# Performance work log

Measured on AMD Instinct MI355X. Metric: run time of the kernel, lower is better.

The kernel has to match this reference:

```python
import jax, jax.numpy as jnp
import numpy as np

B, D, U = 4096, 2048, 2048

def setup_inputs() -> dict:
    key = jax.random.key(0)
    ks = jax.random.split(key, 16)
    s_in = 1.0 / np.sqrt(D)
    s_h = 1.0 / np.sqrt(U)
    inp = {
        "x": jax.random.normal(ks[0], (B, D), jnp.float32),
        "h": jax.random.normal(ks[1], (B, U), jnp.float32),
        "c": jax.random.normal(ks[2], (B, U), jnp.float32),
        # input-to-gate weights (Dense with bias)
        "Wxf": jax.random.normal(ks[3], (D, U), jnp.float32) * s_in,
        "Wxi": jax.random.normal(ks[4], (D, U), jnp.float32) * s_in,
        "Wxo": jax.random.normal(ks[5], (D, U), jnp.float32) * s_in,
        "Wxg": jax.random.normal(ks[6], (D, U), jnp.float32) * s_in,
        "bf": jnp.zeros((U,), jnp.float32),
        "bi": jnp.zeros((U,), jnp.float32),
        "bo": jnp.zeros((U,), jnp.float32),
        "bg": jnp.zeros((U,), jnp.float32),
        # hidden-to-gate weights (no bias)
        "Whf": jax.random.normal(ks[7], (U, U), jnp.float32) * s_h,
        "Whi": jax.random.normal(ks[8], (U, U), jnp.float32) * s_h,
        "Who": jax.random.normal(ks[9], (U, U), jnp.float32) * s_h,
        "Whg": jax.random.normal(ks[10], (U, U), jnp.float32) * s_h,
    }
    return inp

def reference(x, h, c, Wxf, Wxi, Wxo, Wxg, bf, bi, bo, bg, Whf, Whi, Who, Whg):
    # Fuse the 8 small GEMMs into two batched GEMMs over concatenated weights,
    # then one elementwise gate-fusion pass. Math identical to per-Dense form.
    Wx = jnp.concatenate([Wxf, Wxi, Wxo, Wxg], axis=1)   # [D, 4U]
    Wh = jnp.concatenate([Whf, Whi, Who, Whg], axis=1)   # [U, 4U]
    b = jnp.concatenate([bf, bi, bo, bg], axis=0)        # [4U]
    z = x @ Wx + h @ Wh + b                               # [B, 4U]
    zf, zi, zo, zg = jnp.split(z, 4, axis=1)
    f = jax.nn.sigmoid(zf)
    i = jax.nn.sigmoid(zi)
    o = jax.nn.sigmoid(zo)
    g = jnp.tanh(zg)
    c_new = f * c + i * g
    h_new = o * jnp.tanh(c_new)
    return (h_new, c_new)
```

## Files before the change

### kernel.cpp

```cpp
#include <hip/hip_runtime.h>
#include <hip/hip_bf16.h>
#include <stdint.h>

#define B_ 4096
#define D_ 2048
#define U_ 2048
#define K_ 4096
#define N_ 8192

typedef __bf16 bf16x8 __attribute__((ext_vector_type(8)));
typedef float floatx4 __attribute__((ext_vector_type(4)));

__device__ __forceinline__ unsigned short f2bf(float f) {
    union { float f; unsigned int u; } v; v.f = f;
    unsigned int u = v.u;
    unsigned int r = (u + 0x7fffu + ((u >> 16) & 1u)) >> 16;
    return (unsigned short)r;
}

__device__ __forceinline__ float bf2f(unsigned short b) {
    union { unsigned int u; float f; } v;
    v.u = ((unsigned int)b) << 16;
    return v.f;
}

__global__ void k_convA(const float* __restrict__ x, const float* __restrict__ h,
                        unsigned short* __restrict__ Abf) {
    int t = blockIdx.x * blockDim.x + threadIdx.x;
    long e = (long)t * 4;
    int b = (int)(e >> 12);
    int k = (int)(e & 4095);
    const float* src = (k < D_) ? (x + (size_t)b * D_ + k)
                                : (h + (size_t)b * U_ + (k - D_));
    float4 v = *(const float4*)src;
    ushort4 o;
    o.x = f2bf(v.x); o.y = f2bf(v.y); o.z = f2bf(v.z); o.w = f2bf(v.w);
    *(ushort4*)(Abf + e) = o;
}

__global__ void k_convB(const float* __restrict__ Wx0, const float* __restrict__ Wx1,
                        const float* __restrict__ Wx2, const float* __restrict__ Wx3,
                        const float* __restrict__ Wh0, const float* __restrict__ Wh1,
                        const float* __restrict__ Wh2, const float* __restrict__ Wh3,
                        unsigned short* __restrict__ Bt) {
    __shared__ float tile[32][33];
    int g  = blockIdx.z;
    int k0 = blockIdx.x * 32;
    int u0 = blockIdx.y * 32;
    const float* W;
    if (k0 < D_) {
        W = (g == 0 ? Wx0 : g == 1 ? Wx1 : g == 2 ? Wx2 : Wx3) + (size_t)k0 * U_;
    } else {
        W = (g == 0 ? Wh0 : g == 1 ? Wh1 : g == 2 ? Wh2 : Wh3) + (size_t)(k0 - D_) * U_;
    }
    int tx = threadIdx.x & 31, ty = threadIdx.x >> 5;
    #pragma unroll
    for (int j = 0; j < 4; ++j)
        tile[ty + 8 * j][tx] = W[(size_t)(ty + 8 * j) * U_ + u0 + tx];
    __syncthreads();
    #pragma unroll
    for (int j = 0; j < 4; ++j) {
        int u = u0 + ty + 8 * j;
        Bt[(size_t)(g * U_ + u) * K_ + k0 + tx] = f2bf(tile[tx][ty + 8 * j]);
    }
}

__device__ __forceinline__ void gload16(const unsigned short* g, unsigned short* l) {
    __builtin_amdgcn_global_load_lds(
        (const __attribute__((address_space(1))) void*)g,
        (__attribute__((address_space(3))) void*)l, 16, 0, 0);
}

__global__ __launch_bounds__(256) void k_gemm(const unsigned short* __restrict__ A,
                                              const unsigned short* __restrict__ Bt,
                                              unsigned short* __restrict__ Z) {
    __shared__ __align__(16) unsigned short As[128 * 32];
    __shared__ __align__(16) unsigned short Bs[128 * 32];
    const int m0  = blockIdx.y * 128;
    const int n0  = blockIdx.x * 128;
    const int tid = threadIdx.x;
    const int w   = tid >> 6;
    const int l   = tid & 63;

    const unsigned short* gA = A  + (size_t)(m0 + w * 16 + (l >> 2)) * K_ + (l & 3) * 8;
    const unsigned short* gB = Bt + (size_t)(n0 + w * 16 + (l >> 2)) * K_ + (l & 3) * 8;
    unsigned short* lA = As + w * 512;
    unsigned short* lB = Bs + w * 512;

    const int r     = l & 15;
    const int quad  = l >> 4;
    const int m_off = (w & 1) * 64;
    const int n_off = (w >> 1) * 64;

    floatx4 acc[4][4];
    #pragma unroll
    for (int i = 0; i < 4; ++i)
        #pragma unroll
        for (int j = 0; j < 4; ++j)
            #pragma unroll
            for (int e = 0; e < 4; ++e) acc[i][j][e] = 0.f;

    for (int k0 = 0; k0 < K_; k0 += 32) {
        __syncthreads();
        gload16(gA + k0,                  lA);
        gload16(gA + k0 + (size_t)64 * K_, lA + 2048);
        gload16(gB + k0,                  lB);
        gload16(gB + k0 + (size_t)64 * K_, lB + 2048);
        __syncthreads();

        bf16x8 af[4], bfv[4];
        #pragma unroll
        for (int i = 0; i < 4; ++i)
            af[i] = *(const bf16x8*)(As + ((m_off + i * 16 + r) * 32 + quad * 8));
        #pragma unroll
        for (int j = 0; j < 4; ++j)
            bfv[j] = *(const bf16x8*)(Bs + ((n_off + j * 16 + r) * 32 + quad * 8));
        #pragma unroll
        for (int i = 0; i < 4; ++i)
            #pragma unroll
            for (int j = 0; j < 4; ++j)
                acc[i][j] = __builtin_amdgcn_mfma_f32_16x16x32_bf16(
                    af[i], bfv[j], acc[i][j], 0, 0, 0);
    }

    #pragma unroll
    for (int i = 0; i < 4; ++i) {
        #pragma unroll
        for (int j = 0; j < 4; ++j) {
            int col = n0 + n_off + j * 16 + r;
            #pragma unroll
            for (int e = 0; e < 4; ++e) {
                int row = m0 + m_off + i * 16 + quad * 4 + e;
                Z[(size_t)row * N_ + col] = f2bf(acc[i][j][e]);
            }
        }
    }
}

__device__ __forceinline__ float sigmoidf_(float x) { return 1.0f / (1.0f + expf(-x)); }

__global__ void k_gates(const unsigned short* __restrict__ Z, const float* __restrict__ c,
                        const float* __restrict__ bfp, const float* __restrict__ bip,
                        const float* __restrict__ bop, const float* __restrict__ bgp,
                        float* __restrict__ hout, float* __restrict__ cout) {
    int t = blockIdx.x * blockDim.x + threadIdx.x;
    long e = (long)t * 4;
    int b = (int)(e >> 11);
    int u = (int)(e & 2047);
    const size_t zr = (size_t)b * N_;
    ushort4 zf4 = *(const ushort4*)(Z + zr + u);
    ushort4 zi4 = *(const ushort4*)(Z + zr + U_ + u);
    ushort4 zo4 = *(const ushort4*)(Z + zr + 2 * U_ + u);
    ushort4 zg4 = *(const ushort4*)(Z + zr + 3 * U_ + u);
    float4 bfv = *(const float4*)(bfp + u);
    float4 biv = *(const float4*)(bip + u);
    float4 bov = *(const float4*)(bop + u);
    float4 bgv = *(const float4*)(bgp + u);
    float4 cv  = *(const float4*)(c + e);

    float zf[4] = {bf2f(zf4.x), bf2f(zf4.y), bf2f(zf4.z), bf2f(zf4.w)};
    float zi[4] = {bf2f(zi4.x), bf2f(zi4.y), bf2f(zi4.z), bf2f(zi4.w)};
    float zo[4] = {bf2f(zo4.x), bf2f(zo4.y), bf2f(zo4.z), bf2f(zo4.w)};
    float zg[4] = {bf2f(zg4.x), bf2f(zg4.y), bf2f(zg4.z), bf2f(zg4.w)};
    float bff[4] = {bfv.x, bfv.y, bfv.z, bfv.w};
    float bif[4] = {biv.x, biv.y, biv.z, biv.w};
    float bof[4] = {bov.x, bov.y, bov.z, bov.w};
    float bgf[4] = {bgv.x, bgv.y, bgv.z, bgv.w};
    float cf[4]  = {cv.x, cv.y, cv.z, cv.w};

    float4 ho, co;
    float hh[4], cc[4];
    #pragma unroll
    for (int q = 0; q < 4; ++q) {
        float f = sigmoidf_(zf[q] + bff[q]);
        float i = sigmoidf_(zi[q] + bif[q]);
        float o = sigmoidf_(zo[q] + bof[q]);
        float g = tanhf(zg[q] + bgf[q]);
        float cn = f * cf[q] + i * g;
        cc[q] = cn;
        hh[q] = o * tanhf(cn);
    }
    ho.x = hh[0]; ho.y = hh[1]; ho.z = hh[2]; ho.w = hh[3];
    co.x = cc[0]; co.y = cc[1]; co.z = cc[2]; co.w = cc[3];
    *(float4*)(hout + e) = ho;
    *(float4*)(cout + e) = co;
}

extern "C" void kernel_launch(void* const* d_in, const int* in_sizes, int n_in,
                              void* d_out, int out_size, void* d_ws, size_t ws_size,
                              hipStream_t stream) {
    const float* x   = (const float*)d_in[0];
    const float* h   = (const float*)d_in[1];
    const float* c   = (const float*)d_in[2];
    const float* Wxf = (const float*)d_in[3];
    const float* Wxi = (const float*)d_in[4];
    const float* Wxo = (const float*)d_in[5];
    const float* Wxg = (const float*)d_in[6];
    const float* bf  = (const float*)d_in[7];
    const float* bi  = (const float*)d_in[8];
    const float* bo  = (const float*)d_in[9];
    const float* bg  = (const float*)d_in[10];
    const float* Whf = (const float*)d_in[11];
    const float* Whi = (const float*)d_in[12];
    const float* Who = (const float*)d_in[13];
    const float* Whg = (const float*)d_in[14];
    float* out = (float*)d_out;

    unsigned short* Abf = (unsigned short*)d_ws;
    unsigned short* Bt  = Abf + (size_t)B_ * K_;
    unsigned short* Z   = Bt + (size_t)N_ * K_;

    k_convA<<<(B_ * K_ / 4) / 256, 256, 0, stream>>>(x, h, Abf);
    k_convB<<<dim3(K_ / 32, U_ / 32, 4), 256, 0, stream>>>(
        Wxf, Wxi, Wxo, Wxg, Whf, Whi, Who, Whg, Bt);
    k_gemm<<<dim3(N_ / 128, B_ / 128), 256, 0, stream>>>(Abf, Bt, Z);
    k_gates<<<(B_ * U_ / 4) / 256, 256, 0, stream>>>(
        Z, c, bf, bi, bo, bg, out, out + (size_t)B_ * U_);
}
```

Baseline: 593.8 us.

## Vectorize weight transpose, remap GEMM blocks per XCD, use fast gate math

The weight transpose/convert kernel moves to 64x64 tiles with float4 loads and 16-byte bf16 stores, which cuts the number of narrow global transactions. The GEMM grid is flattened and remapped so that each of the 8 XCDs (blocks dispatched round-robin by id) gets a contiguous band of 4 M-tiles, aiming to improve L2 reuse of A and B. The gate kernel replaces expf/tanhf with __expf-based sigmoid and tanh formulas, which are cheaper but slightly less accurate.

```diff
diff --git a/kernel.cpp b/kernel.cpp
--- a/kernel.cpp
+++ b/kernel.cpp
@@ -10,6 +10,7 @@
 
 typedef __bf16 bf16x8 __attribute__((ext_vector_type(8)));
 typedef float floatx4 __attribute__((ext_vector_type(4)));
+typedef unsigned short ushort8 __attribute__((ext_vector_type(8)));
 
 __device__ __forceinline__ unsigned short f2bf(float f) {
     union { float f; unsigned int u; } v; v.f = f;
@@ -22,6 +23,13 @@
     union { unsigned int u; float f; } v;
     v.u = ((unsigned int)b) << 16;
     return v.f;
+}
+
+__device__ __forceinline__ float sigmoid_(float x) {
+    return 1.0f / (1.0f + __expf(-x));
+}
+__device__ __forceinline__ float tanh_(float x) {
+    return 1.0f - 2.0f / (__expf(2.0f * x) + 1.0f);
 }
 
 __global__ void k_convA(const float* __restrict__ x, const float* __restrict__ h,
@@ -38,30 +46,50 @@
     *(ushort4*)(Abf + e) = o;
 }
 
-__global__ void k_convB(const float* __restrict__ Wx0, const float* __restrict__ Wx1,
-                        const float* __restrict__ Wx2, const float* __restrict__ Wx3,
-                        const float* __restrict__ Wh0, const float* __restrict__ Wh1,
-                        const float* __restrict__ Wh2, const float* __restrict__ Wh3,
-                        unsigned short* __restrict__ Bt) {
-    __shared__ float tile[32][33];
-    int g  = blockIdx.z;
-    int k0 = blockIdx.x * 32;
-    int u0 = blockIdx.y * 32;
+__global__ __launch_bounds__(256) void k_convB(
+        const float* __restrict__ Wx0, const float* __restrict__ Wx1,
+        const float* __restrict__ Wx2, const float* __restrict__ Wx3,
+        const float* __restrict__ Wh0, const float* __restrict__ Wh1,
+        const float* __restrict__ Wh2, const float* __restrict__ Wh3,
+        unsigned short* __restrict__ Bt) {
+    __shared__ float tile[64][65];
+    const int g  = blockIdx.z;
+    const int k0 = blockIdx.x * 64;
+    const int u0 = blockIdx.y * 64;
+    const int t  = threadIdx.x;
     const float* W;
     if (k0 < D_) {
         W = (g == 0 ? Wx0 : g == 1 ? Wx1 : g == 2 ? Wx2 : Wx3) + (size_t)k0 * U_;
     } else {
         W = (g == 0 ? Wh0 : g == 1 ? Wh1 : g == 2 ? Wh2 : Wh3) + (size_t)(k0 - D_) * U_;
     }
-    int tx = threadIdx.x & 31, ty = threadIdx.x >> 5;
-    #pragma unroll
-    for (int j = 0; j < 4; ++j)
-        tile[ty + 8 * j][tx] = W[(size_t)(ty + 8 * j) * U_ + u0 + tx];
+    {
+        const int kr_b = t >> 4;
+        const int uc   = (t & 15) * 4;
+        #pragma unroll
+        for (int p = 0; p < 4; ++p) {
+            int kr = p * 16 + kr_b;
+            float4 v = *(const float4*)(W + (size_t)kr * U_ + u0 + uc);
+            tile[kr][uc + 0] = v.x;
+            tile[kr][uc + 1] = v.y;
+            tile[kr][uc + 2] = v.z;
+            tile[kr][uc + 3] = v.w;
+        }
+    }
     __syncthreads();
-    #pragma unroll
-    for (int j = 0; j < 4; ++j) {
-        int u = u0 + ty + 8 * j;
-        Bt[(size_t)(g * U_ + u) * K_ + k0 + tx] = f2bf(tile[tx][ty + 8 * j]);
+    {
+        const int kc = (t & 7) * 8;
+        #pragma unroll
+        for (int p = 0; p < 2; ++p) {
+            int u_idx = p * 32 + (t >> 3);
+            int u = u0 + u_idx;
+            int nrow = g * U_ + u;
+            ushort8 o;
+            #pragma unroll
+            for (int kk = 0; kk < 8; ++kk)
+                o[kk] = f2bf(tile[kc + kk][u_idx]);
+            *(ushort8*)(Bt + (size_t)nrow * K_ + k0 + kc) = o;
+        }
     }
 }
 
@@ -74,10 +102,16 @@
 __global__ __launch_bounds__(256) void k_gemm(const unsigned short* __restrict__ A,
                                               const unsigned short* __restrict__ Bt,
                                               unsigned short* __restrict__ Z) {
+    const int id    = blockIdx.x;
+    const int xcd   = id & 7;
+    const int s     = id >> 3;
+    const int m_blk = (xcd << 2) | (s & 3);
+    const int n_blk = s >> 2;
+    const int m0 = m_blk * 128;
+    const int n0 = n_blk * 128;
+
     __shared__ __align__(16) unsigned short As[128 * 32];
     __shared__ __align__(16) unsigned short Bs[128 * 32];
-    const int m0  = blockIdx.y * 128;
-    const int n0  = blockIdx.x * 128;
     const int tid = threadIdx.x;
     const int w   = tid >> 6;
     const int l   = tid & 63;
@@ -102,9 +136,9 @@
 
     for (int k0 = 0; k0 < K_; k0 += 32) {
         __syncthreads();
-        gload16(gA + k0,                  lA);
+        gload16(gA + k0,                   lA);
         gload16(gA + k0 + (size_t)64 * K_, lA + 2048);
-        gload16(gB + k0,                  lB);
+        gload16(gB + k0,                   lB);
         gload16(gB + k0 + (size_t)64 * K_, lB + 2048);
         __syncthreads();
 
@@ -136,8 +170,6 @@
         }
     }
 }
-
-__device__ __forceinline__ float sigmoidf_(float x) { return 1.0f / (1.0f + expf(-x)); }
 
 __global__ void k_gates(const unsigned short* __restrict__ Z, const float* __restrict__ c,
                         const float* __restrict__ bfp, const float* __restrict__ bip,
@@ -168,18 +200,18 @@
     float bgf[4] = {bgv.x, bgv.y, bgv.z, bgv.w};
     float cf[4]  = {cv.x, cv.y, cv.z, cv.w};
 
-    float4 ho, co;
     float hh[4], cc[4];
     #pragma unroll
     for (int q = 0; q < 4; ++q) {
-        float f = sigmoidf_(zf[q] + bff[q]);
-        float i = sigmoidf_(zi[q] + bif[q]);
-        float o = sigmoidf_(zo[q] + bof[q]);
-        float g = tanhf(zg[q] + bgf[q]);
+        float f = sigmoid_(zf[q] + bff[q]);
+        float i = sigmoid_(zi[q] + bif[q]);
+        float o = sigmoid_(zo[q] + bof[q]);
+        float g = tanh_(zg[q] + bgf[q]);
         float cn = f * cf[q] + i * g;
         cc[q] = cn;
-        hh[q] = o * tanhf(cn);
-    }
+        hh[q] = o * tanh_(cn);
+    }
+    float4 ho, co;
     ho.x = hh[0]; ho.y = hh[1]; ho.z = hh[2]; ho.w = hh[3];
     co.x = cc[0]; co.y = cc[1]; co.z = cc[2]; co.w = cc[3];
     *(float4*)(hout + e) = ho;
@@ -211,9 +243,9 @@
     unsigned short* Z   = Bt + (size_t)N_ * K_;
 
     k_convA<<<(B_ * K_ / 4) / 256, 256, 0, stream>>>(x, h, Abf);
-    k_convB<<<dim3(K_ / 32, U_ / 32, 4), 256, 0, stream>>>(
+    k_convB<<<dim3(K_ / 64, U_ / 64, 4), 256, 0, stream>>>(
         Wxf, Wxi, Wxo, Wxg, Whf, Whi, Who, Whg, Bt);
-    k_gemm<<<dim3(N_ / 128, B_ / 128), 256, 0, stream>>>(Abf, Bt, Z);
+    k_gemm<<<dim3((B_ / 128) * (N_ / 128)), 256, 0, stream>>>(Abf, Bt, Z);
     k_gates<<<(B_ * U_ / 4) / 256, 256, 0, stream>>>(
         Z, c, bf, bi, bo, bg, out, out + (size_t)B_ * U_);
 }
```

After: 605.8 us. +2.0%, slower.
